# Kernel tuning notes

Measured on AMD Instinct MI355X. Metric: run time of the kernel, lower is better.

The kernel has to match this reference:

```python
import jax, jax.numpy as jnp
import numpy as np

EPS = 1e-5  # torch InstanceNorm2d default eps


def conv1x1(x, w, b):
    # x: [B,C,H,W], w: [O,C], b: [O]
    return jnp.einsum('bchw,oc->bohw', x, w) + b[None, :, None, None]


def conv3x3(x, w, b):
    y = jax.lax.conv_general_dilated(x, w, (1, 1), 'SAME',
                                     dimension_numbers=('NCHW', 'OIHW', 'NCHW'))
    return y + b[None, :, None, None]


def inorm(x):
    # InstanceNorm2d, affine=False, biased variance
    m = jnp.mean(x, axis=(2, 3), keepdims=True)
    v = jnp.var(x, axis=(2, 3), keepdims=True)
    return (x - m) * jax.lax.rsqrt(v + EPS)


def self_attn(x, wq, bq, wk, bk, wv, bv, gamma):
    B, C, H, W = x.shape
    N = H * W
    q = conv1x1(x, wq, bq).reshape(B, -1, N)   # [B,C/8,N]
    k = conv1x1(x, wk, bk).reshape(B, -1, N)   # [B,C/8,N]
    A = jax.nn.softmax(jnp.einsum('bdn,bdm->bnm', q, k), axis=-1)  # [B,N,N]
    v = conv1x1(x, wv, bv).reshape(B, C, N)    # [B,C,N]
    out = jnp.einsum('bcm,bnm->bcn', v, A).reshape(B, C, H, W)
    return gamma * out + x


def setup_inputs() -> dict:
    key = jax.random.key(0)
    B, C, H, W = 2, 256, 64, 64
    C8 = C // 8
    ks = iter(jax.random.split(key, 40))

    def n(shape, scale=0.05):
        return jax.random.normal(next(ks), shape, dtype=jnp.float32) * scale

    inp = {
        'x': jax.random.normal(next(ks), (B, C, H, W), dtype=jnp.float32),
        'y': jax.random.normal(next(ks), (B, C, H, W), dtype=jnp.float32),
    }
    for p in ('sa1', 'sa2', 'top'):
        inp[p + '_wq'] = n((C8, C)); inp[p + '_bq'] = n((C8,))
        inp[p + '_wk'] = n((C8, C)); inp[p + '_bk'] = n((C8,))
        inp[p + '_wv'] = n((C, C));  inp[p + '_bv'] = n((C,))
        inp[p + '_gamma'] = n((1,), 0.1)
    inp['conv1_w'] = n((C, C, 3, 3)); inp['conv1_b'] = n((C,))
    inp['conv2_w'] = n((C, C, 3, 3)); inp['conv2_b'] = n((C,))
    return inp


def reference(x, y,
              sa1_wq, sa1_bq, sa1_wk, sa1_bk, sa1_wv, sa1_bv, sa1_gamma,
              sa2_wq, sa2_bq, sa2_wk, sa2_bk, sa2_wv, sa2_bv, sa2_gamma,
              top_wq, top_bq, top_wk, top_bk, top_wv, top_bv, top_gamma,
              conv1_w, conv1_b, conv2_w, conv2_b):
    out_1 = inorm(self_attn(x, sa1_wq, sa1_bq, sa1_wk, sa1_bk, sa1_wv, sa1_bv, sa1_gamma))
    out_2 = inorm(out_1 + conv3x3(out_1, conv1_w, conv1_b))
    out_3 = inorm(self_attn(y, sa2_wq, sa2_bq, sa2_wk, sa2_bk, sa2_wv, sa2_bv, sa2_gamma))

    B, C, H, W = out_2.shape
    N = H * W
    q = conv1x1(out_2, top_wq, top_bq).reshape(B, -1, N)
    k = conv1x1(out_2, top_wk, top_bk).reshape(B, -1, N)
    A = jax.nn.softmax(jnp.einsum('bdn,bdm->bnm', q, k), axis=-1)
    v = conv1x1(out_3, top_wv, top_bv).reshape(B, C, N)
    out = jnp.einsum('bcm,bnm->bcn', v, A).reshape(B, C, H, W)
    out = top_gamma * out + y
    out = inorm(out)
    out = inorm(out + out_3)
    out_4 = conv3x3(out, conv2_w, conv2_b)
    out = inorm(out + out_4)
    return out
```

## Files before the change

kernel.cpp:

```cpp
#include <hip/hip_runtime.h>
#include <hip/hip_bf16.h>

typedef __hip_bfloat16 bf16;
typedef __attribute__((ext_vector_type(8))) short s8v;
typedef __attribute__((ext_vector_type(4))) short s4v;
typedef __attribute__((ext_vector_type(4))) float f4v;

#define NPIX 4096
#define CDIM 256
#define MN_ELEMS (1 << 20)
#define QKVSTR (320L * NPIX)
#define QKTSTR (64L * NPIX)

#if __has_builtin(__builtin_amdgcn_exp2f)
#define EXP2F(x) __builtin_amdgcn_exp2f(x)
#else
#define EXP2F(x) exp2f(x)
#endif

typedef __attribute__((address_space(1))) const unsigned int g_u32;
typedef __attribute__((address_space(3))) unsigned int l_u32;
__device__ __forceinline__ void glds16(const void* g, void* l) {
  __builtin_amdgcn_global_load_lds((g_u32*)g, (l_u32*)l, 16, 0, 0);
}

__device__ inline s8v ld8(const bf16* p) { return *(const s8v*)p; }
__device__ inline s8v ld8(const float* p) {
  float4 f0 = *(const float4*)p;
  float4 f1 = *(const float4*)(p + 4);
  s8v r; bf16* e = (bf16*)&r;
  e[0] = __float2bfloat16(f0.x); e[1] = __float2bfloat16(f0.y);
  e[2] = __float2bfloat16(f0.z); e[3] = __float2bfloat16(f0.w);
  e[4] = __float2bfloat16(f1.x); e[5] = __float2bfloat16(f1.y);
  e[6] = __float2bfloat16(f1.z); e[7] = __float2bfloat16(f1.w);
  return r;
}

__global__ __launch_bounds__(512) void fattn_k(
    const bf16* __restrict__ qkt, const bf16* __restrict__ Vg,
    bf16* __restrict__ out)
{
  __shared__ bf16 k_s[128 * 32];
  __shared__ bf16 v_s[4 * 128 * 32];
  __shared__ bf16 p_s[4 * 64 * 32];
  float* sums = (float*)k_s;

  const int tid = threadIdx.x;
  const int z = blockIdx.z;
  const int w = tid >> 6, lane = tid & 63;
  const int l15 = lane & 15, oct = lane >> 4;
  const int wr2 = w >> 2, wc2 = w & 3;
  const int pc = w >> 1, pn = w & 1;
  const int n0 = blockIdx.x * 64, c0 = blockIdx.y * 128;
  const bf16* qk = qkt + (long)z * QKTSTR;
  const bf16* Vz = Vg + (long)z * QKVSTR;
  const int t2 = tid >> 2, t3 = (tid & 3) * 8;

  if (tid < 256)
    glds16(qk + (long)(n0 + t2) * 64 + t3, p_s + tid * 8);
  glds16(qk + (long)t2 * 64 + 32 + t3, k_s + tid * 8);
  #pragma unroll
  for (int g = 0; g < 4; ++g)
    glds16(Vz + (long)(c0 + t2) * 4096 + g * 32 + t3, v_s + g * 4096 + tid * 8);
  __syncthreads();

  s8v qf[2];
  #pragma unroll
  for (int st = 0; st < 2; ++st)
    qf[st] = *(const s8v*)(p_s + (wr2 * 32 + st * 16 + l15) * 32 + oct * 8);
  __syncthreads();

  f4v acc[2][2];
  #pragma unroll
  for (int i = 0; i < 2; ++i)
    #pragma unroll
    for (int j = 0; j < 2; ++j) acc[i][j] = (f4v){0.f, 0.f, 0.f, 0.f};
  float rs[2] = {0.f, 0.f};

  for (int i = 0; i < 32; ++i) {
    s8v kf[2];
    #pragma unroll
    for (int nt = 0; nt < 2; ++nt)
      kf[nt] = *(const s8v*)(k_s + (wc2 * 32 + nt * 16 + l15) * 32 + oct * 8);
    #pragma unroll
    for (int st = 0; st < 2; ++st) {
      const int n = wr2 * 32 + st * 16 + l15;
      const int sw = ((n >> 1) & 3) << 4;
      f4v sa[2];
      __builtin_amdgcn_s_setprio(1);
      #pragma unroll
      for (int nt = 0; nt < 2; ++nt) {
        f4v zz = (f4v){0.f, 0.f, 0.f, 0.f};
        sa[nt] = __builtin_amdgcn_mfma_f32_16x16x32_bf16(kf[nt], qf[st], zz, 0, 0, 0);
      }
      __builtin_amdgcn_s_setprio(0);
      #pragma unroll
      for (int nt = 0; nt < 2; ++nt) {
        int byte = wc2 * 4096 + n * 64 + nt * 32 + oct * 8;
        byte ^= sw;
        s4v pk; bf16* pe = (bf16*)&pk;
        float rsum = 0.f;
        #pragma unroll
        for (int r = 0; r < 4; ++r) {
          float e = EXP2F(sa[nt][r]);
          rsum += e;
          pe[r] = __float2bfloat16(e);
        }
        rs[st] += rsum;
        *(s4v*)((char*)p_s + byte) = pk;
      }
    }
    __syncthreads();
    #pragma unroll
    for (int kk = 0; kk < 4; ++kk) {
      s8v vf[2], pf[2];
      #pragma unroll
      for (int st = 0; st < 2; ++st)
        vf[st] = *(const s8v*)(v_s + kk * 4096 + (pc * 32 + st * 16 + l15) * 32 + oct * 8);
      #pragma unroll
      for (int nt = 0; nt < 2; ++nt) {
        const int n = pn * 32 + nt * 16 + l15;
        int byte = kk * 4096 + n * 64 + oct * 16;
        byte ^= ((n >> 1) & 3) << 4;
        pf[nt] = *(const s8v*)((const char*)p_s + byte);
      }
      __builtin_amdgcn_s_setprio(1);
      #pragma unroll
      for (int st = 0; st < 2; ++st)
        #pragma unroll
        for (int nt = 0; nt < 2; ++nt)
          acc[st][nt] = __builtin_amdgcn_mfma_f32_16x16x32_bf16(vf[st], pf[nt], acc[st][nt], 0, 0, 0);
      __builtin_amdgcn_s_setprio(0);
    }
    __syncthreads();
    if (i < 31) {
      const int m1 = (i + 1) * 128;
      glds16(qk + (long)(m1 + t2) * 64 + 32 + t3, k_s + tid * 8);
      #pragma unroll
      for (int g = 0; g < 4; ++g)
        glds16(Vz + (long)(c0 + t2) * 4096 + m1 + g * 32 + t3, v_s + g * 4096 + tid * 8);
      __syncthreads();
    }
  }

  #pragma unroll
  for (int st = 0; st < 2; ++st) {
    rs[st] += __shfl_xor(rs[st], 16);
    rs[st] += __shfl_xor(rs[st], 32);
  }
  if (lane < 16) {
    #pragma unroll
    for (int st = 0; st < 2; ++st)
      sums[wc2 * 64 + wr2 * 32 + st * 16 + l15] = rs[st];
  }
  __syncthreads();

  float rinv[2];
  #pragma unroll
  for (int nt = 0; nt < 2; ++nt) {
    const int n = pn * 32 + nt * 16 + l15;
    rinv[nt] = 1.f / (sums[n] + sums[64 + n] + sums[128 + n] + sums[192 + n]);
  }
  bf16* op = out + (long)z * ((long)CDIM * NPIX);
  #pragma unroll
  for (int st = 0; st < 2; ++st) {
    const int gc = c0 + pc * 32 + st * 16 + oct * 4;
    #pragma unroll
    for (int nt = 0; nt < 2; ++nt) {
      const int gn = n0 + pn * 32 + nt * 16 + l15;
      #pragma unroll
      for (int r = 0; r < 4; ++r)
        op[(long)(gc + r) * NPIX + gn] = __float2bfloat16(acc[st][nt][r] * rinv[nt]);
    }
  }
}

__global__ __launch_bounds__(512) void conv_k(
    const bf16* __restrict__ x, const bf16* __restrict__ wcvt,
    const float* __restrict__ bias, bf16* __restrict__ out)
{
  __shared__ bf16 lds[3 * 66 * 66];
  const int tid = threadIdx.x;
  const int h = blockIdx.x;
  const int o0 = blockIdx.y * 128;
  x   += (long)blockIdx.z * CDIM * NPIX;
  out += (long)blockIdx.z * CDIM * NPIX;

  const int w = tid >> 6, lane = tid & 63;
  const int l15 = lane & 15, oct = lane >> 4;

  if (tid < 192) {
    int row = tid >> 6, c = tid & 63;
    lds[(row * 66 + 0) * 66 + c] = __float2bfloat16(0.f);
    lds[(row * 66 + 65) * 66 + c] = __float2bfloat16(0.f);
  }

  f4v acc[4];
  #pragma unroll
  for (int nf = 0; nf < 4; ++nf) acc[nf] = (f4v){0.f, 0.f, 0.f, 0.f};

  const int w2 = tid & 31, chi = tid >> 5;
  const long arow = (long)(o0 + w * 16 + l15) * 2304;

  for (int cg = 0; cg < 4; ++cg) {
    __syncthreads();
    #pragma unroll
    for (int it = 0; it < 12; ++it) {
      int row = it >> 2, cgi = it & 3;
      int c = cgi * 16 + chi;
      int hh = h + row - 1;
      unsigned int pix = 0;
      if ((unsigned)hh < 64u)
        pix = *(const unsigned int*)(x + (long)(cg * 64 + c) * 4096 + hh * 64 + w2 * 2);
      const bf16* pp = (const bf16*)&pix;
      lds[(row * 66 + (w2 * 2 + 1)) * 66 + c] = pp[0];
      lds[(row * 66 + (w2 * 2 + 2)) * 66 + c] = pp[1];
    }
    __syncthreads();

    #pragma unroll
    for (int j = 0; j < 9; ++j) {
      const int dy = j / 3, dx = j % 3;
      #pragma unroll
      for (int kc = 0; kc < 2; ++kc) {
        s8v af = *(const s8v*)(wcvt + arow + j * 256 + cg * 64 + kc * 32 + oct * 8);
        s8v bfv[4];
        #pragma unroll
        for (int nf = 0; nf < 4; ++nf)
          bfv[nf] = *(const s8v*)&lds[(dy * 66 + (nf * 16 + l15 + dx)) * 66 + kc * 32 + oct * 8];
        #pragma unroll
        for (int nf = 0; nf < 4; ++nf)
          acc[nf] = __builtin_amdgcn_mfma_f32_16x16x32_bf16(af, bfv[nf], acc[nf], 0, 0, 0);
      }
    }
  }

  #pragma unroll
  for (int nf = 0; nf < 4; ++nf) {
    const int gn = h * 64 + nf * 16 + l15;
    const int go = o0 + w * 16 + oct * 4;
    #pragma unroll
    for (int r = 0; r < 4; ++r)
      out[(long)(go + r) * NPIX + gn] = __float2bfloat16(acc[nf][r] + bias[go + r]);
  }
}

template<int QKT, typename TBe>
__global__ __launch_bounds__(256) void proj_k(
    const float* __restrict__ A, const float* __restrict__ A2,
    const TBe* __restrict__ B1, const TBe* __restrict__ B2,
    const float* __restrict__ bias, const float* __restrict__ bias2,
    bf16* __restrict__ Cm, bf16* __restrict__ qkt,
    int M, int N, int K, long bbat, long cbat, int nchunk)
{
  __shared__ bf16 a_s[64][40];
  __shared__ bf16 b_s[64][40];
  const int tid = threadIdx.x;
  const int z = blockIdx.z, stage = z >> 1, bat = z & 1;
  const float* Au = stage ? A2 : A;
  const float* biasu = stage ? bias2 : bias;
  const TBe* Bm = (stage ? B2 : B1) + bat * bbat;
  Cm += z * cbat;
  if (QKT) qkt += z * QKTSTR;
  const int m0 = blockIdx.y * 64, n0 = blockIdx.x * 64;
  const int w = tid >> 6, lane = tid & 63;
  const int l15 = lane & 15, oct = lane >> 4;

  f4v acc[4];
  #pragma unroll
  for (int i = 0; i < 4; ++i) acc[i] = (f4v){0.f, 0.f, 0.f, 0.f};

  const int a_i0 = tid >> 2, a_i1 = (tid & 3) * 8;
  const int b_i0 = tid >> 3, b_i1 = (tid & 7) * 8;

  s8v pa, pb;
  auto ldA = [&](int kc, s8v& d) {
    if (m0 + a_i0 < M) d = ld8(Au + (long)(m0 + a_i0) * K + kc * 32 + a_i1);
    else d = (s8v){0,0,0,0,0,0,0,0};
  };
  auto ldB = [&](int kc, s8v& d) {
    d = ld8(Bm + (long)(kc * 32 + b_i0) * N + n0 + b_i1);
  };

  ldA(0, pa); ldB(0, pb);
  for (int kc = 0; kc < nchunk; ++kc) {
    *(s8v*)&a_s[a_i0][a_i1] = pa;
    {
      const bf16* e = (const bf16*)&pb;
      #pragma unroll
      for (int j = 0; j < 8; ++j) b_s[b_i1 + j][b_i0] = e[j];
    }
    __syncthreads();
    if (kc + 1 < nchunk) { ldA(kc + 1, pa); ldB(kc + 1, pb); }
    s8v af = *(const s8v*)&a_s[w * 16 + l15][oct * 8];
    #pragma unroll
    for (int nt = 0; nt < 4; ++nt) {
      s8v bfr = *(const s8v*)&b_s[nt * 16 + l15][oct * 8];
      acc[nt] = __builtin_amdgcn_mfma_f32_16x16x32_bf16(af, bfr, acc[nt], 0, 0, 0);
    }
    __syncthreads();
  }
  const int gm_base = m0 + w * 16 + oct * 4;
  #pragma unroll
  for (int nt = 0; nt < 4; ++nt) {
    const int gn = n0 + nt * 16 + l15;
    #pragma unroll
    for (int r = 0; r < 4; ++r) {
      int gm = gm_base + r;
      if (gm < M) {
        float vv = acc[nt][r] + biasu[gm];
        if (QKT && gm < 64) {
          float vv2 = (gm < 32) ? vv * 1.44269504f : vv;
          qkt[(long)gn * 64 + gm] = __float2bfloat16(vv2);
        } else {
          Cm[(long)gm * N + gn] = __float2bfloat16(vv);
        }
      }
    }
  }
}

__global__ __launch_bounds__(256) void cat_k(
    const float* __restrict__ wq, const float* __restrict__ bq,
    const float* __restrict__ wk, const float* __restrict__ bk,
    const float* __restrict__ wv, const float* __restrict__ bv,
    float* __restrict__ wcat, float* __restrict__ bcat, int M)
{
  int idx = blockIdx.x * 256 + threadIdx.x;
  int total = M << 8;
  if (idx < total) {
    int r = idx >> 8, c = idx & 255;
    float v;
    if (r < 32) v = wq[r * 256 + c];
    else if (r < 64) v = wk[(r - 32) * 256 + c];
    else v = wv[(r - 64) * 256 + c];
    wcat[idx] = v;
  } else if (idx < total + M) {
    int r = idx - total;
    bcat[r] = (r < 32) ? bq[r] : (r < 64) ? bk[r - 32] : bv[r - 64];
  }
}

__global__ __launch_bounds__(256) void cvtw2_k(
    const float* __restrict__ w1, const float* __restrict__ w2,
    bf16* __restrict__ o1, bf16* __restrict__ o2)
{
  const float* in = blockIdx.y ? w2 : w1;
  bf16* out = blockIdx.y ? o2 : o1;
  int idx = blockIdx.x * 256 + threadIdx.x;
  int o = idx / 2304, r = idx % 2304;
  int j = r >> 8, c = r & 255;
  out[idx] = __float2bfloat16(in[(o * 256 + c) * 9 + j]);
}

__device__ inline void ld16(const bf16* p, float* v) {
  s8v r0 = *(const s8v*)p, r1 = *(const s8v*)(p + 8);
  const bf16* e0 = (const bf16*)&r0; const bf16* e1 = (const bf16*)&r1;
  #pragma unroll
  for (int j = 0; j < 8; ++j) { v[j] = __bfloat162float(e0[j]); v[8 + j] = __bfloat162float(e1[j]); }
}
__device__ inline void ld16(const float* p, float* v) {
  #pragma unroll
  for (int q = 0; q < 4; ++q) {
    float4 f = *(const float4*)(p + q * 4);
    v[q * 4 + 0] = f.x; v[q * 4 + 1] = f.y; v[q * 4 + 2] = f.z; v[q * 4 + 3] = f.w;
  }
}
__device__ inline void st16(bf16* p, const float* v) {
  s8v o0, o1v; bf16* f0 = (bf16*)&o0; bf16* f1 = (bf16*)&o1v;
  #pragma unroll
  for (int j = 0; j < 8; ++j) { f0[j] = __float2bfloat16(v[j]); f1[j] = __float2bfloat16(v[8 + j]); }
  *(s8v*)p = o0; *(s8v*)(p + 8) = o1v;
}
__device__ inline void st16(float* p, const float* v) {
  #pragma unroll
  for (int q = 0; q < 4; ++q) {
    float4 f; f.x = v[q * 4 + 0]; f.y = v[q * 4 + 1]; f.z = v[q * 4 + 2]; f.w = v[q * 4 + 3];
    *(float4*)(p + q * 4) = f;
  }
}

template<typename TAe, typename TBe, typename TOe, int G>
__global__ __launch_bounds__(256) void inorm_k(
    const TAe* __restrict__ a, const TBe* __restrict__ b,
    const float* __restrict__ g, TOe* __restrict__ out)
{
  __shared__ float red[8];
  const int tid = threadIdx.x;
  const long base = (long)blockIdx.x * NPIX + tid * 16;
  float gv = G ? *g : 1.f;
  float va[16], vbv[16], v[16];
  ld16(a + base, va);
  ld16(b + base, vbv);
  #pragma unroll
  for (int j = 0; j < 16; ++j) v[j] = gv * va[j] + vbv[j];
  float sum = 0.f, sq = 0.f;
  #pragma unroll
  for (int j = 0; j < 16; ++j) { sum += v[j]; sq += v[j] * v[j]; }
  #pragma unroll
  for (int s = 32; s; s >>= 1) { sum += __shfl_xor(sum, s); sq += __shfl_xor(sq, s); }
  if ((tid & 63) == 0) { red[tid >> 6] = sum; red[4 + (tid >> 6)] = sq; }
  __syncthreads();
  sum = red[0] + red[1] + red[2] + red[3];
  sq  = red[4] + red[5] + red[6] + red[7];
  float mean = sum * (1.f / NPIX);
  float var  = fmaxf(sq * (1.f / NPIX) - mean * mean, 0.f);
  float rstd = rsqrtf(var + 1e-5f);
  float o[16];
  #pragma unroll
  for (int j = 0; j < 16; ++j) o[j] = (v[j] - mean) * rstd;
  st16(out + base, o);
}

static const long CN = (long)CDIM * NPIX;

static void attn_core(int nb, bf16* qkv, bf16* qkt, bf16* t0, hipStream_t stream)
{
  fattn_k<<<dim3(64, 2, nb), dim3(512), 0, stream>>>(qkt, qkv + 64 * NPIX, t0);
}

static void run_conv(const bf16* src, const bf16* wcvt, const float* cb,
                     bf16* dst, hipStream_t stream)
{
  conv_k<<<dim3(64, 2, 2), dim3(512), 0, stream>>>(src, wcvt, cb, dst);
}

extern "C" void kernel_launch(void* const* d_in, const int* in_sizes, int n_in,
                              void* d_out, int out_size, void* d_ws, size_t ws_size,
                              hipStream_t stream)
{
  (void)in_sizes; (void)n_in; (void)out_size; (void)ws_size;
  const float* x = (const float*)d_in[0];
  const float* y = (const float*)d_in[1];
  auto W = [&](int i) { return (const float*)d_in[i]; };

  char* wp = (char*)d_ws;
  auto take = [&](size_t nbytes) { char* p = wp; wp += (nbytes + 255) & ~(size_t)255; return p; };
  bf16*  qkv   = (bf16*)take((size_t)4 * QKVSTR * 2);
  bf16*  qkt   = (bf16*)take((size_t)4 * QKTSTR * 2);
  bf16*  t0    = (bf16*)take((size_t)4 * CN * 2);
  bf16*  u1    = (bf16*)take(2 * CN * 2);
  bf16*  u2    = (bf16*)take(2 * CN * 2);
  bf16*  u3    = (bf16*)take(2 * CN * 2);
  bf16*  u4    = (bf16*)take(2 * CN * 2);
  bf16*  wcvt1 = (bf16*)take((size_t)589824 * 2);
  bf16*  wcvt2 = (bf16*)take((size_t)589824 * 2);
  float* wcat1 = (float*)take((size_t)81920 * 4);
  float* bcat1 = (float*)take(320 * 4);
  float* wcat2 = (float*)take((size_t)81920 * 4);
  float* bcat2 = (float*)take(320 * 4);
  float* wqk   = (float*)take((size_t)16384 * 4);
  float* bqk   = (float*)take(64 * 4);
  bf16*  cvout = qkv;

  dim3 TB(256);

  cat_k<<<dim3(322), TB, 0, stream>>>(W(2), W(3), W(4), W(5), W(6), W(7), wcat1, bcat1, 320);
  cat_k<<<dim3(322), TB, 0, stream>>>(W(9), W(10), W(11), W(12), W(13), W(14), wcat2, bcat2, 320);
  cat_k<<<dim3(65),  TB, 0, stream>>>(W(16), W(17), W(18), W(19), nullptr, nullptr, wqk, bqk, 64);
  cvtw2_k<<<dim3(2304, 2), TB, 0, stream>>>(W(23), W(25), wcvt1, wcvt2);

  proj_k<1,float><<<dim3(64,5,4), TB, 0, stream>>>(
      wcat1, wcat2, x, y, bcat1, bcat2, qkv, qkt, 320, NPIX, 256, CN, QKVSTR, 8);
  attn_core(4, qkv, qkt, t0, stream);

  inorm_k<bf16,float,bf16,1><<<dim3(512), TB, 0, stream>>>(t0, x, W(8), u1);
  inorm_k<bf16,float,bf16,1><<<dim3(512), TB, 0, stream>>>(t0 + 2 * CN, y, W(15), u3);

  run_conv(u1, wcvt1, W(24), cvout, stream);
  inorm_k<bf16,bf16,bf16,0><<<dim3(512), TB, 0, stream>>>(u1, cvout, nullptr, u2);

  proj_k<1,bf16><<<dim3(64,1,2), TB, 0, stream>>>(
      wqk, wqk, u2, u2, bqk, bqk, qkv, qkt, 64, NPIX, 256, CN, QKVSTR, 8);
  proj_k<0,bf16><<<dim3(64,4,2), TB, 0, stream>>>(
      W(20), W(20), u3, u3, W(21), W(21), qkv + 64 * NPIX, qkt, 256, NPIX, 256, CN, QKVSTR, 8);
  attn_core(2, qkv, qkt, t0, stream);
  inorm_k<bf16,float,bf16,1><<<dim3(512), TB, 0, stream>>>(t0, y, W(22), u1);
  inorm_k<bf16,bf16,bf16,0><<<dim3(512), TB, 0, stream>>>(u1, u3, nullptr, u4);
  run_conv(u4, wcvt2, W(26), cvout, stream);
  inorm_k<bf16,bf16,float,0><<<dim3(512), TB, 0, stream>>>(u4, cvout, nullptr, (float*)d_out);
}
```

Before: 366.7 us.

## Template attention kernel on channel tile and XOR-swizzle K/V/Q LDS layouts

Makes the flash-attention kernel's channel tile a template parameter. When the batch count is 2 it launches a 64-channel tile variant with twice as many blocks, aiming to fill more CUs. It also applies an XOR swizzle to the K, Q and V staging writes and the matching LDS reads to reduce bank conflicts. The smaller tile recomputes QK^T and softmax exponentials twice as often per pixel block.

```diff
diff --git a/kernel.cpp b/kernel.cpp
--- a/kernel.cpp
+++ b/kernel.cpp
@@ -36,12 +36,14 @@
   return r;
 }
 
+template<int CB>
 __global__ __launch_bounds__(512) void fattn_k(
     const bf16* __restrict__ qkt, const bf16* __restrict__ Vg,
     bf16* __restrict__ out)
 {
+  constexpr int SC = CB / 64;
   __shared__ bf16 k_s[128 * 32];
-  __shared__ bf16 v_s[4 * 128 * 32];
+  __shared__ bf16 v_s[4 * CB * 32];
   __shared__ bf16 p_s[4 * 64 * 32];
   float* sums = (float*)k_s;
 
@@ -51,28 +53,46 @@
   const int l15 = lane & 15, oct = lane >> 4;
   const int wr2 = w >> 2, wc2 = w & 3;
   const int pc = w >> 1, pn = w & 1;
-  const int n0 = blockIdx.x * 64, c0 = blockIdx.y * 128;
+  const int n0 = blockIdx.x * 64, c0 = blockIdx.y * CB;
   const bf16* qk = qkt + (long)z * QKTSTR;
   const bf16* Vz = Vg + (long)z * QKVSTR;
-  const int t2 = tid >> 2, t3 = (tid & 3) * 8;
+
+  const int t2 = tid >> 2;
+  const int kq3 = ((tid & 3) ^ ((t2 >> 1) & 3)) * 8;
+  const int vrow = t2 & (CB - 1);
+  const int vq3 = ((tid & 3) ^ ((vrow >> 1) & 3)) * 8;
+
+  auto stageK = [&](int m) {
+    glds16(qk + (long)(m + t2) * 64 + 32 + kq3, k_s + tid * 8);
+  };
+  auto stageV = [&](int m) {
+    #pragma unroll
+    for (int it = 0; it < CB / 32; ++it) {
+      const int flat = it * 4096 + tid * 8;
+      const int g = flat / (CB * 32);
+      glds16(Vz + (long)(c0 + vrow) * 4096 + m + g * 32 + vq3, v_s + flat);
+    }
+  };
 
   if (tid < 256)
-    glds16(qk + (long)(n0 + t2) * 64 + t3, p_s + tid * 8);
-  glds16(qk + (long)t2 * 64 + 32 + t3, k_s + tid * 8);
-  #pragma unroll
-  for (int g = 0; g < 4; ++g)
-    glds16(Vz + (long)(c0 + t2) * 4096 + g * 32 + t3, v_s + g * 4096 + tid * 8);
+    glds16(qk + (long)(n0 + t2) * 64 + kq3, p_s + tid * 8);
+  stageK(0);
+  stageV(0);
   __syncthreads();
 
   s8v qf[2];
   #pragma unroll
-  for (int st = 0; st < 2; ++st)
-    qf[st] = *(const s8v*)(p_s + (wr2 * 32 + st * 16 + l15) * 32 + oct * 8);
+  for (int st = 0; st < 2; ++st) {
+    const int row = wr2 * 32 + st * 16 + l15;
+    int byte = row * 64 + oct * 16;
+    byte ^= ((row >> 1) & 3) << 4;
+    qf[st] = *(const s8v*)((const char*)p_s + byte);
+  }
   __syncthreads();
 
-  f4v acc[2][2];
-  #pragma unroll
-  for (int i = 0; i < 2; ++i)
+  f4v acc[SC][2];
+  #pragma unroll
+  for (int i = 0; i < SC; ++i)
     #pragma unroll
     for (int j = 0; j < 2; ++j) acc[i][j] = (f4v){0.f, 0.f, 0.f, 0.f};
   float rs[2] = {0.f, 0.f};
@@ -80,8 +100,12 @@
   for (int i = 0; i < 32; ++i) {
     s8v kf[2];
     #pragma unroll
-    for (int nt = 0; nt < 2; ++nt)
-      kf[nt] = *(const s8v*)(k_s + (wc2 * 32 + nt * 16 + l15) * 32 + oct * 8);
+    for (int nt = 0; nt < 2; ++nt) {
+      const int row = wc2 * 32 + nt * 16 + l15;
+      int byte = row * 64 + oct * 16;
+      byte ^= ((row >> 1) & 3) << 4;
+      kf[nt] = *(const s8v*)((const char*)k_s + byte);
+    }
     #pragma unroll
     for (int st = 0; st < 2; ++st) {
       const int n = wr2 * 32 + st * 16 + l15;
@@ -113,10 +137,14 @@
     __syncthreads();
     #pragma unroll
     for (int kk = 0; kk < 4; ++kk) {
-      s8v vf[2], pf[2];
-      #pragma unroll
-      for (int st = 0; st < 2; ++st)
-        vf[st] = *(const s8v*)(v_s + kk * 4096 + (pc * 32 + st * 16 + l15) * 32 + oct * 8);
+      s8v vf[SC], pf[2];
+      #pragma unroll
+      for (int st = 0; st < SC; ++st) {
+        const int row = pc * (CB / 4) + st * 16 + l15;
+        int byte = kk * (CB * 64) + row * 64 + oct * 16;
+        byte ^= ((row >> 1) & 3) << 4;
+        vf[st] = *(const s8v*)((const char*)v_s + byte);
+      }
       #pragma unroll
       for (int nt = 0; nt < 2; ++nt) {
         const int n = pn * 32 + nt * 16 + l15;
@@ -126,7 +154,7 @@
       }
       __builtin_amdgcn_s_setprio(1);
       #pragma unroll
-      for (int st = 0; st < 2; ++st)
+      for (int st = 0; st < SC; ++st)
         #pragma unroll
         for (int nt = 0; nt < 2; ++nt)
           acc[st][nt] = __builtin_amdgcn_mfma_f32_16x16x32_bf16(vf[st], pf[nt], acc[st][nt], 0, 0, 0);
@@ -135,10 +163,8 @@
     __syncthreads();
     if (i < 31) {
       const int m1 = (i + 1) * 128;
-      glds16(qk + (long)(m1 + t2) * 64 + 32 + t3, k_s + tid * 8);
-      #pragma unroll
-      for (int g = 0; g < 4; ++g)
-        glds16(Vz + (long)(c0 + t2) * 4096 + m1 + g * 32 + t3, v_s + g * 4096 + tid * 8);
+      stageK(m1);
+      stageV(m1);
       __syncthreads();
     }
   }
@@ -163,8 +189,8 @@
   }
   bf16* op = out + (long)z * ((long)CDIM * NPIX);
   #pragma unroll
-  for (int st = 0; st < 2; ++st) {
-    const int gc = c0 + pc * 32 + st * 16 + oct * 4;
+  for (int st = 0; st < SC; ++st) {
+    const int gc = c0 + pc * (CB / 4) + st * 16 + oct * 4;
     #pragma unroll
     for (int nt = 0; nt < 2; ++nt) {
       const int gn = n0 + pn * 32 + nt * 16 + l15;
@@ -416,7 +442,10 @@
 
 static void attn_core(int nb, bf16* qkv, bf16* qkt, bf16* t0, hipStream_t stream)
 {
-  fattn_k<<<dim3(64, 2, nb), dim3(512), 0, stream>>>(qkt, qkv + 64 * NPIX, t0);
+  if (nb == 4)
+    fattn_k<128><<<dim3(64, 2, 4), dim3(512), 0, stream>>>(qkt, qkv + 64 * NPIX, t0);
+  else
+    fattn_k<64><<<dim3(64, 4, 2), dim3(512), 0, stream>>>(qkt, qkv + 64 * NPIX, t0);
 }
 
 static void run_conv(const bf16* src, const bf16* wcvt, const float* cb,
```

Result: faster. 355.9 us (-2.9%).
